# Optimization experiments

Hardware: AMD Instinct MI355X
Metric: run time of the kernel (lower is better)

Reference implementation:

```python
import jax, jax.numpy as jnp
import numpy as np

B, L, CIN, DLOI, NPTS0, NPTS1, H = 2, 5000, 256, 128, 32, 8, 256
HALF = DLOI // 2
EPS = 1e-5


def _bn_params(k, c):
    k1, k2, k3, k4 = jax.random.split(k, 4)
    gamma = 1.0 + 0.1 * jax.random.normal(k1, (c,), jnp.float32)
    beta = 0.1 * jax.random.normal(k2, (c,), jnp.float32)
    mean = 0.1 * jax.random.normal(k3, (c,), jnp.float32)
    var = 0.5 + jax.random.uniform(k4, (c,), jnp.float32)
    return jnp.stack([gamma, beta, mean, var])  # [4, c]


def setup_inputs():
    key = jax.random.key(0)
    ks = jax.random.split(key, 12)
    feature = jax.random.normal(ks[0], (B, CIN, H, H), jnp.float32)
    lines = jax.random.uniform(ks[1], (B, L, 2, 2), jnp.float32, minval=0.0, maxval=255.0)
    w_fc1 = 0.05 * jax.random.normal(ks[2], (DLOI, CIN), jnp.float32)
    b_fc1 = jnp.zeros((DLOI,), jnp.float32)
    bn1 = _bn_params(ks[3], DLOI)
    c1_w = 0.1 * jax.random.normal(ks[4], (HALF, DLOI), jnp.float32)
    c1_b = jnp.zeros((HALF,), jnp.float32)
    bn2 = _bn_params(ks[5], HALF)
    c2_w = 0.1 * jax.random.normal(ks[6], (HALF, HALF, 3), jnp.float32)
    c2_b = jnp.zeros((HALF,), jnp.float32)
    bn3 = _bn_params(ks[7], HALF)
    c3_w = 0.1 * jax.random.normal(ks[8], (DLOI, HALF), jnp.float32)
    c3_b = jnp.zeros((DLOI,), jnp.float32)
    w_fc2 = 0.03 * jax.random.normal(ks[9], (4, DLOI * NPTS1), jnp.float32)
    b_fc2 = jnp.zeros((4,), jnp.float32)
    return {"feature": feature, "lines": lines, "w_fc1": w_fc1, "b_fc1": b_fc1,
            "bn1": bn1, "c1_w": c1_w, "c1_b": c1_b, "bn2": bn2, "c2_w": c2_w,
            "c2_b": c2_b, "bn3": bn3, "c3_w": c3_w, "c3_b": c3_b,
            "w_fc2": w_fc2, "b_fc2": b_fc2}


def _bn(v, p):
    # v: [N, C, P], p: [4, C] = gamma, beta, running_mean, running_var (eval mode)
    scale = (p[0] * jax.lax.rsqrt(p[3] + EPS))[None, :, None]
    shift = p[1][None, :, None]
    return (v - p[2][None, :, None]) * scale + shift


def _forward(feature, lines, w_fc1, b_fc1, bn1, c1_w, c1_b, bn2, c2_w, c2_b,
             bn3, c3_w, c3_b, w_fc2, b_fc2):
    # fc1: 1x1 conv over backbone feature -> [B, DLOI, H, H]
    x = jnp.einsum('bchw,oc->bohw', feature, w_fc1) + b_fc1[None, :, None, None]

    # sample NPTS0 points along each line: p = p0*lam + p1*(1-lam) - 0.5
    lam = jnp.linspace(0.0, 1.0, NPTS0, dtype=jnp.float32)[:, None]  # [NPTS0, 1]
    p = lines[:, :, 0:1, :] * lam + lines[:, :, 1:2, :] * (1.0 - lam) - 0.5  # [B,L,NPTS0,2]
    px, py = p[..., 0], p[..., 1]
    px0 = jnp.clip(jnp.floor(px), 0.0, H - 1.0)
    py0 = jnp.clip(jnp.floor(py), 0.0, H - 1.0)
    px1 = jnp.clip(px0 + 1.0, 0.0, H - 1.0)
    py1 = jnp.clip(py0 + 1.0, 0.0, H - 1.0)
    i0, j0 = px0.astype(jnp.int32), py0.astype(jnp.int32)
    i1, j1 = px1.astype(jnp.int32), py1.astype(jnp.int32)
    w00 = (px1 - px) * (py1 - py)
    w10 = (px - px0) * (py1 - py)
    w01 = (px1 - px) * (py - py0)
    w11 = (px - px0) * (py - py0)

    def gather_one(feat, i0b, j0b, i1b, j1b, a, b, c, d):
        # feat [C,H,W]; indices/weights [L, NPTS0] -> [C, L, NPTS0]
        return (feat[:, i0b, j0b] * a + feat[:, i1b, j0b] * b
                + feat[:, i0b, j1b] * c + feat[:, i1b, j1b] * d)

    xp = jax.vmap(gather_one)(x, i0, j0, i1, j1, w00, w10, w01, w11)  # [B,C,L,NPTS0]
    xp = xp.transpose(0, 2, 1, 3).reshape(B * L, DLOI, NPTS0)

    # MaxPool1d(kernel=4, stride=4): NPTS0 -> NPTS1
    xp = xp.reshape(B * L, DLOI, NPTS1, NPTS0 // NPTS1).max(-1)

    # Bottleneck1D (eval-mode BN): x + op(x)
    h = jax.nn.relu(_bn(xp, bn1))
    h = jnp.einsum('ncp,oc->nop', h, c1_w) + c1_b[None, :, None]
    h = jax.nn.relu(_bn(h, bn2))
    h = jax.lax.conv_general_dilated(h, c2_w, window_strides=(1,), padding=((1, 1),),
                                     dimension_numbers=('NCH', 'OIH', 'NCH')) + c2_b[None, :, None]
    h = jax.nn.relu(_bn(h, bn3))
    h = jnp.einsum('ncp,oc->nop', h, c3_w) + c3_b[None, :, None]
    y = xp + h

    # fc2: ReLU + Linear(DLOI*NPTS1 -> 4), then softmax scores
    flat = y.reshape(B * L, DLOI * NPTS1)
    logits = jax.nn.relu(flat) @ w_fc2.T + b_fc2
    s = jax.nn.softmax(logits, axis=-1)
    return s


def reference(feature, lines, w_fc1, b_fc1, bn1, c1_w, c1_b, bn2, c2_w, c2_b,
              bn3, c3_w, c3_b, w_fc2, b_fc2):
    return _forward(feature, lines, w_fc1, b_fc1, bn1, c1_w, c1_b, bn2, c2_w,
                    c2_b, bn3, c3_w, c3_b, w_fc2, b_fc2)
```

## Files before the change

kernel.cpp:

```cpp
#include <hip/hip_runtime.h>
#include <math.h>
#include <stdint.h>

#define HH 256
#define LPB 5000

typedef _Float16 h2v  __attribute__((ext_vector_type(2)));
typedef _Float16 f16x8 __attribute__((ext_vector_type(8)));
typedef float    f32x4 __attribute__((ext_vector_type(4)));

__device__ __forceinline__ h2v u2h(unsigned int u) { return __builtin_bit_cast(h2v, u); }
__device__ __forceinline__ unsigned int h2u(h2v h) { return __builtin_bit_cast(unsigned int, h); }

__device__ __forceinline__ float fdot2(h2v a, unsigned int w, float c) {
#if __has_builtin(__builtin_amdgcn_fdot2)
    return __builtin_amdgcn_fdot2(a, u2h(w), c, false);
#else
    h2v b = u2h(w);
    return c + (float)a[0] * (float)b[0] + (float)a[1] * (float)b[1];
#endif
}

__device__ __forceinline__ h2v relu2(h2v a) {
    h2v z = (h2v)(_Float16)0.f;
#if __has_builtin(__builtin_elementwise_max)
    return __builtin_elementwise_max(a, z);
#else
    h2v r; r[0] = a[0] > z[0] ? a[0] : z[0]; r[1] = a[1] > z[1] ? a[1] : z[1]; return r;
#endif
}
__device__ __forceinline__ h2v hmax2v(h2v a, h2v b) {
#if __has_builtin(__builtin_elementwise_max)
    return __builtin_elementwise_max(a, b);
#else
    h2v r; r[0] = a[0] > b[0] ? a[0] : b[0]; r[1] = a[1] > b[1] ? a[1] : b[1]; return r;
#endif
}

__global__ __launch_bounds__(256) void prep_small(
    const float* __restrict__ w_fc1, const float* __restrict__ c1w,
    const float* __restrict__ c2w,  const float* __restrict__ c3w,
    const float* __restrict__ wfc2, const float* __restrict__ bn1,
    const float* __restrict__ bn2,  const float* __restrict__ bn3,
    _Float16* __restrict__ wf16, _Float16* __restrict__ w1r,
    _Float16* __restrict__ w2r, _Float16* __restrict__ w3r,
    unsigned int* __restrict__ wfc2p, unsigned int* __restrict__ bn_pk)
{
    int i = blockIdx.x * 256 + threadIdx.x;
    if (i < 32768) { wf16[i] = (_Float16)w_fc1[i]; return; }
    i -= 32768;
    if (i < 8192) {
        w1r[i] = (_Float16)c1w[i]; return;
    }
    i -= 8192;
    if (i < 12288) {
        int ii = i & 63, o = (i >> 6) & 63, tap = i >> 12;
        w2r[i] = (_Float16)c2w[(o * 64 + ii) * 3 + tap]; return;
    }
    i -= 12288;
    if (i < 8192) {
        w3r[i] = (_Float16)c3w[i]; return;
    }
    i -= 8192;
    if (i < 2048) {
        int c2 = i & 63, p = (i >> 6) & 7, j = i >> 9;
        h2v v = { (_Float16)wfc2[j * 1024 + (2 * c2) * 8 + p],
                  (_Float16)wfc2[j * 1024 + (2 * c2 + 1) * 8 + p] };
        wfc2p[(j * 8 + p) * 64 + c2] = h2u(v); return;
    }
    i -= 2048;
    if (i < 128) {
        const float* bn; int C, base, hcount;
        if (i < 64)      { bn = bn1; C = 128; base = 0;   hcount = 64; }
        else if (i < 96) { bn = bn2; C = 64;  base = 128; hcount = 32; i -= 64; }
        else             { bn = bn3; C = 64;  base = 192; hcount = 32; i -= 96; }
        int c0 = 2 * i, c1 = 2 * i + 1;
        float s0 = bn[c0] * rsqrtf(bn[3 * C + c0] + 1e-5f);
        float s1 = bn[c1] * rsqrtf(bn[3 * C + c1] + 1e-5f);
        float h0 = bn[C + c0] - bn[2 * C + c0] * s0;
        float h1 = bn[C + c1] - bn[2 * C + c1] * s1;
        h2v sv = { (_Float16)s0, (_Float16)s1 };
        h2v hv = { (_Float16)h0, (_Float16)h1 };
        bn_pk[base + i] = h2u(sv);
        bn_pk[base + hcount + i] = h2u(hv);
    }
}

__global__ __launch_bounds__(256, 4) void fc1_fused(
    const float* __restrict__ feat,
    const _Float16* __restrict__ W,
    const float* __restrict__ bias,
    unsigned int* __restrict__ X)
{
    __shared__ _Float16 Th[128 * 40];
    __shared__ _Float16 Wl[128 * 40];
    const int t = threadIdx.x;
    const int lane = t & 63, wave = t >> 6;
    const int wm = wave & 1, wn = wave >> 1;
    const int l15 = lane & 15, kg = lane >> 4;
    const int pix0g = blockIdx.x << 7;
    const int b = blockIdx.x >> 9;
    const int pix0l = pix0g & 65535;
    const float* fbase = feat + (size_t)b * (256u * 65536u) + pix0l;

    const int sc4 = (t & 7) * 4;
    const int sp  = (t >> 3) * 4;

    f32x4 acc[4][4];
#pragma unroll
    for (int a = 0; a < 4; a++)
#pragma unroll
        for (int c = 0; c < 4; c++) acc[a][c] = (f32x4)0.f;

    for (int ks = 0; ks < 8; ks++) {
        const int k0 = ks * 32;
        __syncthreads();
        float vv[4][4];
#pragma unroll
        for (int cc = 0; cc < 4; cc++)
            *(float4*)&vv[cc][0] =
                *(const float4*)(fbase + (size_t)(k0 + sc4 + cc) * 65536 + sp);
#pragma unroll
        for (int p = 0; p < 4; p++) {
            h2v lo = { (_Float16)vv[0][p], (_Float16)vv[1][p] };
            h2v hi = { (_Float16)vv[2][p], (_Float16)vv[3][p] };
            uint2 u = { h2u(lo), h2u(hi) };
            *(uint2*)&Th[(sp + p) * 40 + sc4] = u;
        }
#pragma unroll
        for (int r = 0; r < 2; r++) {
            int idx = t + r * 256;
            int row = idx >> 2, ko = (idx & 3) * 8;
            *(uint4*)&Wl[row * 40 + ko] = *(const uint4*)(W + row * 256 + k0 + ko);
        }
        __syncthreads();
        f16x8 af[4], bf[4];
#pragma unroll
        for (int mt = 0; mt < 4; mt++)
            af[mt] = *(const f16x8*)&Wl[(wm * 64 + mt * 16 + l15) * 40 + kg * 8];
#pragma unroll
        for (int nt = 0; nt < 4; nt++)
            bf[nt] = *(const f16x8*)&Th[(wn * 64 + nt * 16 + l15) * 40 + kg * 8];
#pragma unroll
        for (int mt = 0; mt < 4; mt++)
#pragma unroll
            for (int nt = 0; nt < 4; nt++)
                acc[mt][nt] = __builtin_amdgcn_mfma_f32_16x16x32_f16(af[mt], bf[nt], acc[mt][nt], 0, 0, 0);
    }
#pragma unroll
    for (int mt = 0; mt < 4; mt++) {
        int o = wm * 64 + mt * 16 + (lane >> 4) * 4;
        float4 b4 = *(const float4*)(bias + o);
#pragma unroll
        for (int nt = 0; nt < 4; nt++) {
            int pix = pix0g + wn * 64 + nt * 16 + (lane & 15);
            f32x4 a = acc[mt][nt];
            h2v lo = { (_Float16)(a[0] + b4.x), (_Float16)(a[1] + b4.y) };
            h2v hi = { (_Float16)(a[2] + b4.z), (_Float16)(a[3] + b4.w) };
            uint2 v = { h2u(lo), h2u(hi) };
            *(uint2*)(X + (size_t)pix * 64 + (o >> 1)) = v;
        }
    }
}

__global__ __launch_bounds__(256, 4) void line_v4(
    const unsigned int* __restrict__ X,
    const float* __restrict__ lines,
    const _Float16* __restrict__ w1r, const float* __restrict__ c1b,
    const _Float16* __restrict__ w2r, const float* __restrict__ c2b,
    const _Float16* __restrict__ w3r, const float* __restrict__ c3b,
    const unsigned int* __restrict__ wfc2p, const float* __restrict__ bfc2,
    const unsigned int* __restrict__ bn_pk,
    float* __restrict__ out)
{
    __shared__ int geoB[256];
    __shared__ unsigned int geoWA[256], geoWB[256];
    __shared__ unsigned int xp[64 * 68];
    __shared__ unsigned int abuf[64 * 68];
    __shared__ float red[128];

    const int t = threadIdx.x;
    const int n0 = blockIdx.x * 8;
    const int lane = t & 63;
    const int w = t >> 6;
    const int l15 = lane & 15;
    const int kg = lane >> 4;
    const int ko8 = kg * 8;

    {
        int l = t >> 5, k = t & 31;
        int n = n0 + l;
        float4 ln = *(const float4*)(lines + n * 4);
        float lam = (float)k / 31.0f;
        float px = ln.x * lam + ln.z * (1.f - lam) - 0.5f;
        float py = ln.y * lam + ln.w * (1.f - lam) - 0.5f;
        float px0 = fminf(fmaxf(floorf(px), 0.f), 255.f);
        float py0 = fminf(fmaxf(floorf(py), 0.f), 255.f);
        float dx = px - px0, dy = py - py0;
        float ex = 1.f - dx, ey = 1.f - dy;
        h2v wA = { (_Float16)(ex * ey), (_Float16)(dx * ey) };
        h2v wB = { (_Float16)(ex * dy), (_Float16)(dx * dy) };
        int b = (n >= LPB) ? 1 : 0;
        int pixflat = (b << 16) + ((int)px0 << 8) + (int)py0;
        geoB[t] = pixflat << 6;
        geoWA[t] = h2u(wA); geoWB[t] = h2u(wB);
    }
    __syncthreads();

    {
        const int c8 = t & 15;
        const int sub = t >> 4;
        const int line = sub >> 1;
        const int gbase = (sub & 1) * 4;
        const uint4* xq = (const uint4*)X;
        uint4 s1 = *(const uint4*)(bn_pk + c8 * 4);
        uint4 h1 = *(const uint4*)(bn_pk + 64 + c8 * 4);
#pragma unroll
        for (int lg = 0; lg < 4; lg++) {
            int g = gbase + lg;
            int ptb = line * 32 + g * 4;
            h2v m0, m1, m2, m3;
#pragma unroll
            for (int s = 0; s < 4; s++) {
                int pt = ptb + s;
                int base4 = (geoB[pt] >> 2) + c8;
                h2v wA = u2h(geoWA[pt]), wB = u2h(geoWB[pt]);
                uint4 q00 = xq[base4];
                uint4 q10 = xq[base4 + 4096];
                uint4 q01 = xq[base4 + 16];
                uint4 q11 = xq[base4 + 4112];
                h2v w00 = { wA[0], wA[0] }, w10 = { wA[1], wA[1] };
                h2v w01 = { wB[0], wB[0] }, w11 = { wB[1], wB[1] };
                h2v v0 = u2h(q00.x) * w00 + u2h(q10.x) * w10 + u2h(q01.x) * w01 + u2h(q11.x) * w11;
                h2v v1 = u2h(q00.y) * w00 + u2h(q10.y) * w10 + u2h(q01.y) * w01 + u2h(q11.y) * w11;
                h2v v2 = u2h(q00.z) * w00 + u2h(q10.z) * w10 + u2h(q01.z) * w01 + u2h(q11.z) * w11;
                h2v v3 = u2h(q00.w) * w00 + u2h(q10.w) * w10 + u2h(q01.w) * w01 + u2h(q11.w) * w11;
                if (s == 0) { m0 = v0; m1 = v1; m2 = v2; m3 = v3; }
                else { m0 = hmax2v(m0, v0); m1 = hmax2v(m1, v1);
                       m2 = hmax2v(m2, v2); m3 = hmax2v(m3, v3); }
            }
            int colw = line * 8 + g;
            uint4 raw = { h2u(m0), h2u(m1), h2u(m2), h2u(m3) };
            *(uint4*)&xp[colw * 68 + c8 * 4] = raw;
            h2v r0 = relu2(m0 * u2h(s1.x) + u2h(h1.x));
            h2v r1 = relu2(m1 * u2h(s1.y) + u2h(h1.y));
            h2v r2 = relu2(m2 * u2h(s1.z) + u2h(h1.z));
            h2v r3 = relu2(m3 * u2h(s1.w) + u2h(h1.w));
            uint4 act = { h2u(r0), h2u(r1), h2u(r2), h2u(r3) };
            *(uint4*)&abuf[colw * 68 + c8 * 4] = act;
        }
    }
    __syncthreads();

    f32x4 acc1[4];
#pragma unroll
    for (int nt = 0; nt < 4; nt++) acc1[nt] = (f32x4)0.f;
    {
        const int o = w * 16 + l15;
        f16x8 af[4];
#pragma unroll
        for (int kt = 0; kt < 4; kt++)
            af[kt] = *(const f16x8*)(w1r + o * 128 + kt * 32 + ko8);
#pragma unroll
        for (int nt = 0; nt < 4; nt++) {
            const int colb = nt * 16 + l15;
#pragma unroll
            for (int kt = 0; kt < 4; kt++) {
                f16x8 bf = *(const f16x8*)&abuf[colb * 68 + kt * 16 + kg * 4];
                acc1[nt] = __builtin_amdgcn_mfma_f32_16x16x32_f16(af[kt], bf, acc1[nt], 0, 0, 0);
            }
        }
    }
    __syncthreads();

    {
        float4 b1 = *(const float4*)(c1b + w * 16 + kg * 4);
        const int o2 = w * 8 + kg * 2;
        h2v sA = u2h(bn_pk[128 + o2]), sB = u2h(bn_pk[128 + o2 + 1]);
        h2v hA = u2h(bn_pk[160 + o2]), hB = u2h(bn_pk[160 + o2 + 1]);
#pragma unroll
        for (int nt = 0; nt < 4; nt++) {
            const int col = nt * 16 + l15;
            const int colp = (col >> 3) * 10 + 1 + (col & 7);
            h2v v0 = { (_Float16)(acc1[nt][0] + b1.x), (_Float16)(acc1[nt][1] + b1.y) };
            h2v v1 = { (_Float16)(acc1[nt][2] + b1.z), (_Float16)(acc1[nt][3] + b1.w) };
            v0 = relu2(v0 * sA + hA);
            v1 = relu2(v1 * sB + hB);
            uint2 u = { h2u(v0), h2u(v1) };
            *(uint2*)&abuf[colp * 36 + o2] = u;
        }
#pragma unroll
        for (int e = 0; e < 2; e++) {
            int idx = t * 2 + e;
            int pc = idx >> 5, i2 = idx & 31;
            int pl = pc >> 1, side = pc & 1;
            abuf[(pl * 10 + side * 9) * 36 + i2] = 0;
        }
    }
    __syncthreads();

    f32x4 acc2[4];
#pragma unroll
    for (int nt = 0; nt < 4; nt++) acc2[nt] = (f32x4)0.f;
    {
        const int o = w * 16 + l15;
        const int colp0 = (l15 >> 3) * 10 + 1 + (l15 & 7);
#pragma unroll
        for (int tap = 0; tap < 3; tap++) {
            f16x8 wa0 = *(const f16x8*)(w2r + (tap * 64 + o) * 64 + ko8);
            f16x8 wa1 = *(const f16x8*)(w2r + (tap * 64 + o) * 64 + 32 + ko8);
#pragma unroll
            for (int nt = 0; nt < 4; nt++) {
                const int cp = colp0 + nt * 20 + tap - 1;
                f16x8 b0 = *(const f16x8*)&abuf[cp * 36 + kg * 4];
                f16x8 b1 = *(const f16x8*)&abuf[cp * 36 + 16 + kg * 4];
                acc2[nt] = __builtin_amdgcn_mfma_f32_16x16x32_f16(wa0, b0, acc2[nt], 0, 0, 0);
                acc2[nt] = __builtin_amdgcn_mfma_f32_16x16x32_f16(wa1, b1, acc2[nt], 0, 0, 0);
            }
        }
    }
    __syncthreads();

    {
        float4 b2 = *(const float4*)(c2b + w * 16 + kg * 4);
        const int o2 = w * 8 + kg * 2;
        h2v sA = u2h(bn_pk[192 + o2]), sB = u2h(bn_pk[192 + o2 + 1]);
        h2v hA = u2h(bn_pk[224 + o2]), hB = u2h(bn_pk[224 + o2 + 1]);
#pragma unroll
        for (int nt = 0; nt < 4; nt++) {
            const int col = nt * 16 + l15;
            h2v v0 = { (_Float16)(acc2[nt][0] + b2.x), (_Float16)(acc2[nt][1] + b2.y) };
            h2v v1 = { (_Float16)(acc2[nt][2] + b2.z), (_Float16)(acc2[nt][3] + b2.w) };
            v0 = relu2(v0 * sA + hA);
            v1 = relu2(v1 * sB + hB);
            uint2 u = { h2u(v0), h2u(v1) };
            *(uint2*)&abuf[col * 36 + o2] = u;
        }
    }
    __syncthreads();

    {
#pragma unroll
        for (int mi = 0; mi < 2; mi++) {
            const int om = (2 * w + mi) * 16 + l15;
            f16x8 af0 = *(const f16x8*)(w3r + om * 64 + ko8);
            f16x8 af1 = *(const f16x8*)(w3r + om * 64 + 32 + ko8);
            f32x4 acc3[4];
#pragma unroll
            for (int nt = 0; nt < 4; nt++) acc3[nt] = (f32x4)0.f;
#pragma unroll
            for (int nt = 0; nt < 4; nt++) {
                const int col = nt * 16 + l15;
                f16x8 b0 = *(const f16x8*)&abuf[col * 36 + kg * 4];
                f16x8 b1 = *(const f16x8*)&abuf[col * 36 + 16 + kg * 4];
                acc3[nt] = __builtin_amdgcn_mfma_f32_16x16x32_f16(af0, b0, acc3[nt], 0, 0, 0);
                acc3[nt] = __builtin_amdgcn_mfma_f32_16x16x32_f16(af1, b1, acc3[nt], 0, 0, 0);
            }
            float4 b3 = *(const float4*)(c3b + (2 * w + mi) * 16 + kg * 4);
            const int o2 = (2 * w + mi) * 8 + kg * 2;
#pragma unroll
            for (int nt = 0; nt < 4; nt++) {
                const int col = nt * 16 + l15;
                uint2 xv = *(const uint2*)&xp[col * 68 + o2];
                h2v y0 = { (_Float16)(acc3[nt][0] + b3.x), (_Float16)(acc3[nt][1] + b3.y) };
                h2v y1 = { (_Float16)(acc3[nt][2] + b3.z), (_Float16)(acc3[nt][3] + b3.w) };
                y0 = relu2(u2h(xv.x) + y0);
                y1 = relu2(u2h(xv.y) + y1);
                uint2 u = { h2u(y0), h2u(y1) };
                *(uint2*)&xp[col * 68 + o2] = u;
            }
        }
    }
    __syncthreads();

    {
        const int og = w;
        const int col = t & 63;
        const int obH = __builtin_amdgcn_readfirstlane(og * 16);
        const int p = col & 7, l = col >> 3;
        h2v yv[16];
#pragma unroll
        for (int j = 0; j < 16; j++) yv[j] = u2h(xp[col * 68 + obH + j]);
        float aj[4] = { 0.f, 0.f, 0.f, 0.f };
#pragma unroll
        for (int j = 0; j < 4; j++) {
            unsigned int wv2[16];
#pragma unroll
            for (int q = 0; q < 4; q++)
                *(uint4*)&wv2[q * 4] = *(const uint4*)(wfc2p + (j * 8 + p) * 64 + obH + q * 4);
#pragma unroll
            for (int j16 = 0; j16 < 16; j16++) aj[j] = fdot2(yv[j16], wv2[j16], aj[j]);
        }
#pragma unroll
        for (int off = 4; off > 0; off >>= 1) {
#pragma unroll
            for (int j = 0; j < 4; j++) aj[j] += __shfl_down(aj[j], off, 8);
        }
        if ((t & 7) == 0) {
#pragma unroll
            for (int j = 0; j < 4; j++) red[og * 32 + l * 4 + j] = aj[j];
        }
    }
    __syncthreads();

    if (t < 8) {
        float lg[4];
#pragma unroll
        for (int j = 0; j < 4; j++)
            lg[j] = bfc2[j] + red[t * 4 + j] + red[32 + t * 4 + j]
                  + red[64 + t * 4 + j] + red[96 + t * 4 + j];
        float mx = fmaxf(fmaxf(lg[0], lg[1]), fmaxf(lg[2], lg[3]));
        float e0 = expf(lg[0] - mx), e1 = expf(lg[1] - mx);
        float e2 = expf(lg[2] - mx), e3 = expf(lg[3] - mx);
        float s = 1.f / (e0 + e1 + e2 + e3);
        float4 r = { e0 * s, e1 * s, e2 * s, e3 * s };
        *(float4*)(out + (size_t)(n0 + t) * 4) = r;
    }
}

extern "C" void kernel_launch(void* const* d_in, const int* in_sizes, int n_in,
                              void* d_out, int out_size, void* d_ws, size_t ws_size,
                              hipStream_t stream) {
    const float* feature = (const float*)d_in[0];
    const float* lines   = (const float*)d_in[1];
    const float* w_fc1   = (const float*)d_in[2];
    const float* b_fc1   = (const float*)d_in[3];
    const float* bn1     = (const float*)d_in[4];
    const float* c1_w    = (const float*)d_in[5];
    const float* c1_b    = (const float*)d_in[6];
    const float* bn2     = (const float*)d_in[7];
    const float* c2_w    = (const float*)d_in[8];
    const float* c2_b    = (const float*)d_in[9];
    const float* bn3     = (const float*)d_in[10];
    const float* c3_w    = (const float*)d_in[11];
    const float* c3_b    = (const float*)d_in[12];
    const float* w_fc2   = (const float*)d_in[13];
    const float* b_fc2   = (const float*)d_in[14];
    float* out = (float*)d_out;

    char* ws = (char*)d_ws;
    unsigned int* X     = (unsigned int*)ws;
    _Float16*     wf16  = (_Float16*)(ws + 33554432);
    _Float16*     w1r   = (_Float16*)(ws + 33619968);
    _Float16*     w2r   = (_Float16*)(ws + 33636352);
    _Float16*     w3r   = (_Float16*)(ws + 33660928);
    unsigned int* wfc2p = (unsigned int*)(ws + 33677312);
    unsigned int* bn_pk = (unsigned int*)(ws + 33685504);

    prep_small<<<249, 256, 0, stream>>>(w_fc1, c1_w, c2_w, c3_w, w_fc2, bn1, bn2, bn3,
                                        wf16, w1r, w2r, w3r, wfc2p, bn_pk);
    fc1_fused<<<1024, 256, 0, stream>>>(feature, wf16, b_fc1, X);
    line_v4<<<1250, 256, 0, stream>>>(X, lines, w1r, c1_b, w2r, c2_b,
                                      w3r, c3_b, wfc2p, b_fc2, bn_pk, out);
}
```

Measured before the change: 269.3 us.

## Double-buffer fc1 shared tiles to overlap global loads with MFMA

The fc1 GEMM kernel now uses two LDS buffers for feature and weight tiles, issuing global loads for the next K-slice into registers before the MFMA compute of the current slice and writing them to LDS afterward. This removes one barrier per iteration and hides global load latency behind matrix math. It doubles LDS use, holds more prefetch registers, and lowers the launch-bounds occupancy hint from 4 to 3 blocks per CU.

```diff
diff --git a/kernel.cpp b/kernel.cpp
--- a/kernel.cpp
+++ b/kernel.cpp
@@ -86,14 +86,14 @@
     }
 }
 
-__global__ __launch_bounds__(256, 4) void fc1_fused(
+__global__ __launch_bounds__(256, 3) void fc1_fused(
     const float* __restrict__ feat,
     const _Float16* __restrict__ W,
     const float* __restrict__ bias,
     unsigned int* __restrict__ X)
 {
-    __shared__ _Float16 Th[128 * 40];
-    __shared__ _Float16 Wl[128 * 40];
+    __shared__ _Float16 Th[2][128 * 40];
+    __shared__ _Float16 Wl[2][128 * 40];
     const int t = threadIdx.x;
     const int lane = t & 63, wave = t >> 6;
     const int wm = wave & 1, wn = wave >> 1;
@@ -105,47 +105,58 @@
 
     const int sc4 = (t & 7) * 4;
     const int sp  = (t >> 3) * 4;
-
-    f32x4 acc[4][4];
-#pragma unroll
-    for (int a = 0; a < 4; a++)
-#pragma unroll
-        for (int c = 0; c < 4; c++) acc[a][c] = (f32x4)0.f;
-
-    for (int ks = 0; ks < 8; ks++) {
+    const int wr0 = t >> 2, wko = (t & 3) * 8;
+
+    float vv[4][4];
+    uint4 wv[2];
+
+    auto gload = [&](int ks) {
         const int k0 = ks * 32;
-        __syncthreads();
-        float vv[4][4];
 #pragma unroll
         for (int cc = 0; cc < 4; cc++)
             *(float4*)&vv[cc][0] =
                 *(const float4*)(fbase + (size_t)(k0 + sc4 + cc) * 65536 + sp);
+        wv[0] = *(const uint4*)(W + wr0 * 256 + k0 + wko);
+        wv[1] = *(const uint4*)(W + (64 + wr0) * 256 + k0 + wko);
+    };
+    auto swrite = [&](int bb) {
 #pragma unroll
         for (int p = 0; p < 4; p++) {
             h2v lo = { (_Float16)vv[0][p], (_Float16)vv[1][p] };
             h2v hi = { (_Float16)vv[2][p], (_Float16)vv[3][p] };
             uint2 u = { h2u(lo), h2u(hi) };
-            *(uint2*)&Th[(sp + p) * 40 + sc4] = u;
-        }
-#pragma unroll
-        for (int r = 0; r < 2; r++) {
-            int idx = t + r * 256;
-            int row = idx >> 2, ko = (idx & 3) * 8;
-            *(uint4*)&Wl[row * 40 + ko] = *(const uint4*)(W + row * 256 + k0 + ko);
-        }
+            *(uint2*)&Th[bb][(sp + p) * 40 + sc4] = u;
+        }
+        *(uint4*)&Wl[bb][wr0 * 40 + wko] = wv[0];
+        *(uint4*)&Wl[bb][(64 + wr0) * 40 + wko] = wv[1];
+    };
+
+    f32x4 acc[4][4];
+#pragma unroll
+    for (int a = 0; a < 4; a++)
+#pragma unroll
+        for (int c = 0; c < 4; c++) acc[a][c] = (f32x4)0.f;
+
+    gload(0);
+    swrite(0);
+#pragma unroll
+    for (int ks = 0; ks < 8; ks++) {
         __syncthreads();
+        if (ks < 7) gload(ks + 1);
+        const int bb = ks & 1;
         f16x8 af[4], bf[4];
 #pragma unroll
         for (int mt = 0; mt < 4; mt++)
-            af[mt] = *(const f16x8*)&Wl[(wm * 64 + mt * 16 + l15) * 40 + kg * 8];
+            af[mt] = *(const f16x8*)&Wl[bb][(wm * 64 + mt * 16 + l15) * 40 + kg * 8];
 #pragma unroll
         for (int nt = 0; nt < 4; nt++)
-            bf[nt] = *(const f16x8*)&Th[(wn * 64 + nt * 16 + l15) * 40 + kg * 8];
+            bf[nt] = *(const f16x8*)&Th[bb][(wn * 64 + nt * 16 + l15) * 40 + kg * 8];
 #pragma unroll
         for (int mt = 0; mt < 4; mt++)
 #pragma unroll
             for (int nt = 0; nt < 4; nt++)
                 acc[mt][nt] = __builtin_amdgcn_mfma_f32_16x16x32_f16(af[mt], bf[nt], acc[mt][nt], 0, 0, 0);
+        if (ks < 7) swrite((ks + 1) & 1);
     }
 #pragma unroll
     for (int mt = 0; mt < 4; mt++) {
```

Result: slower. 278.6 us (+3.5%).
